# Performance work log

Measured on AMD Instinct MI355X. Metric: run time of the kernel, lower is better.

Reference implementation:

```python
import jax, jax.numpy as jnp
import numpy as np

H = 64

def _lstm_cell(x, h, c, Wih, Whh, bih, bhh):
    # x: [B, in], h/c: [B, H]; gate order i, f, g, o (PyTorch convention)
    g = x @ Wih.T + h @ Whh.T + (bih + bhh)
    i, f, gg, o = jnp.split(g, 4, axis=-1)
    i = jax.nn.sigmoid(i)
    f = jax.nn.sigmoid(f)
    gg = jnp.tanh(gg)
    o = jax.nn.sigmoid(o)
    c_new = f * c + i * gg
    h_new = o * jnp.tanh(c_new)
    return h_new, c_new


def setup_inputs() -> dict:
    key = jax.random.key(0)
    ks = jax.random.split(key, 12)
    B, T = 512, 1024
    s1 = 1.0 / np.sqrt(H)
    u = lambda k, shape: jax.random.uniform(k, shape, jnp.float32, -s1, s1)
    return {
        "x": jax.random.normal(ks[0], (B, T), jnp.float32),
        "W_ih1": u(ks[1], (4 * H, 1)),
        "W_hh1": u(ks[2], (4 * H, H)),
        "b_ih1": u(ks[3], (4 * H,)),
        "b_hh1": u(ks[4], (4 * H,)),
        "W_ih2": u(ks[5], (4 * H, H)),
        "W_hh2": u(ks[6], (4 * H, H)),
        "b_ih2": u(ks[7], (4 * H,)),
        "b_hh2": u(ks[8], (4 * H,)),
        "W_l": u(ks[9], (1, H)),
        "b_l": u(ks[10], (1,)),
        "future": 64,
    }


def reference(x, W_ih1, W_hh1, b_ih1, b_hh1, W_ih2, W_hh2, b_ih2, b_hh2, W_l, b_l, future):
    B, T = x.shape
    h1 = jnp.zeros((B, H), jnp.float32)
    c1 = jnp.zeros((B, H), jnp.float32)
    h2 = jnp.zeros((B, H), jnp.float32)
    c2 = jnp.zeros((B, H), jnp.float32)

    def step(carry, xt):
        h1, c1, h2, c2 = carry
        h1, c1 = _lstm_cell(xt, h1, c1, W_ih1, W_hh1, b_ih1, b_hh1)
        h2, c2 = _lstm_cell(h1, h2, c2, W_ih2, W_hh2, b_ih2, b_hh2)
        out = h2 @ W_l.T + b_l  # [B, 1]
        return (h1, c1, h2, c2), out

    xs = x.T[:, :, None]  # [T, B, 1]
    (h1, c1, h2, c2), outs = jax.lax.scan(step, (h1, c1, h2, c2), xs)
    last_out = outs[-1]  # [B, 1]

    def fstep(carry, _):
        h1, c1, h2, c2, out = carry
        h1, c1 = _lstm_cell(out, h1, c1, W_ih1, W_hh1, b_ih1, b_hh1)
        h2, c2 = _lstm_cell(h1, h2, c2, W_ih2, W_hh2, b_ih2, b_hh2)
        out = h2 @ W_l.T + b_l
        return (h1, c1, h2, c2, out), out

    if future > 0:
        _, fouts = jax.lax.scan(fstep, (h1, c1, h2, c2, last_out), None, length=future)
        outs = jnp.concatenate([outs, fouts], axis=0)  # [T+future, B, 1]

    return outs[:, :, 0].T  # [B, T+future]
```

## Files before the change

kernel.cpp:

```cpp
#include <hip/hip_runtime.h>

#define TMAIN 1024
#define TFUT  64
#define TTOT  (TMAIN + TFUT)

#define RL(v,k) __uint_as_float(__builtin_amdgcn_readlane(__float_as_uint(v),(k)))
#define DPPF(v,ctrl) __int_as_float(__builtin_amdgcn_update_dpp(0, __float_as_int(v), (ctrl), 0xf, 0xf, true))
#define DPPADD(d,ctrl,rm) d += __int_as_float(__builtin_amdgcn_update_dpp(0, __float_as_int(d), (ctrl), (rm), 0xf, true));

#define LD16(N,P) \
  float4 N##0=(P)[0],  N##1=(P)[1],  N##2=(P)[2],  N##3=(P)[3],  \
         N##4=(P)[4],  N##5=(P)[5],  N##6=(P)[6],  N##7=(P)[7],  \
         N##8=(P)[8],  N##9=(P)[9],  N##10=(P)[10], N##11=(P)[11], \
         N##12=(P)[12], N##13=(P)[13], N##14=(P)[14], N##15=(P)[15];

#define PIN(v) asm volatile("" : "+v"(v.x), "+v"(v.y), "+v"(v.z), "+v"(v.w));
#define PIN16(N) PIN(N##0) PIN(N##1) PIN(N##2) PIN(N##3) PIN(N##4) PIN(N##5) PIN(N##6) PIN(N##7) \
                 PIN(N##8) PIN(N##9) PIN(N##10) PIN(N##11) PIN(N##12) PIN(N##13) PIN(N##14) PIN(N##15)

#define D4(W,k,hv) \
  a0 = fmaf(RL(hv,(k)+0), W.x, a0); \
  a1 = fmaf(RL(hv,(k)+1), W.y, a1); \
  a2 = fmaf(RL(hv,(k)+2), W.z, a2); \
  a3 = fmaf(RL(hv,(k)+3), W.w, a3);

#define DOT64(N,hv) \
  D4(N##0,0,hv)   D4(N##1,4,hv)   D4(N##2,8,hv)   D4(N##3,12,hv)  \
  D4(N##4,16,hv)  D4(N##5,20,hv)  D4(N##6,24,hv)  D4(N##7,28,hv)  \
  D4(N##8,32,hv)  D4(N##9,36,hv)  D4(N##10,40,hv) D4(N##11,44,hv) \
  D4(N##12,48,hv) D4(N##13,52,hv) D4(N##14,56,hv) D4(N##15,60,hv)

__global__ __launch_bounds__(256, 2)
void lstm2_kernel(const float* __restrict__ x,
                  const float* __restrict__ Wih1,
                  const float* __restrict__ Whh1,
                  const float* __restrict__ bih1,
                  const float* __restrict__ bhh1,
                  const float* __restrict__ Wih2,
                  const float* __restrict__ Whh2,
                  const float* __restrict__ bih2,
                  const float* __restrict__ bhh2,
                  const float* __restrict__ Wl,
                  const float* __restrict__ bl,
                  float* __restrict__ out)
{
    const int b    = blockIdx.x;
    const int tid  = threadIdx.x;
    const int wv   = tid >> 6;
    const int lane = tid & 63;
    const int q    = lane & 3;
    const int unit = (wv << 4) | (lane >> 2);
    const int row  = (q << 6) | unit;

    LD16(A, reinterpret_cast<const float4*>(Whh1 + row * 64))
    LD16(C, reinterpret_cast<const float4*>(Wih2 + row * 64))
    LD16(D, reinterpret_cast<const float4*>(Whh2 + row * 64))
    PIN16(A) PIN16(C) PIN16(D)

    const float wih1r = Wih1[row];
    const float bias1 = bih1[row] + bhh1[row];
    const float bias2 = bih2[row] + bhh2[row];
    const float wl_l  = Wl[lane];
    const float bl0   = bl[0];

    __shared__ float h1buf[64];
    __shared__ float h2buf[64];

    float vh1o = 0.0f, vh2o = 0.0f, c1 = 0.0f, c2 = 0.0f, xv = 0.0f;
    const float* xb = x + b * TMAIN;
    float* ob = out + b * TTOT;

    for (int s = 0; s < TTOT; ++s) {
        const float x_t = (s < TMAIN) ? xb[s] : xv;

        float a0 = 0.f, a1 = 0.f, a2 = 0.f, a3 = 0.f;
        DOT64(A, vh1o)
        float acc = fmaf(wih1r, x_t, bias1) + ((a0 + a1) + (a2 + a3));

        float earg = (q == 2) ? -2.0f * acc : -acc;
        float r  = 1.0f / (1.0f + __expf(earg));
        float gv = (q == 2) ? 2.0f * r - 1.0f : r;
        float p1v = DPPF(gv, 0xB1);
        float p2v = DPPF(gv, 0x4E);
        float p3v = DPPF(gv, 0x1B);
        float gi = (q==0)?gv : (q==1)?p1v : (q==2)?p2v : p3v;
        float gf = (q==1)?gv : (q==0)?p1v : (q==3)?p2v : p3v;
        float gg = (q==2)?gv : (q==3)?p1v : (q==0)?p2v : p3v;
        float go = (q==3)?gv : (q==2)?p1v : (q==1)?p2v : p3v;
        c1 = fmaf(gf, c1, gi * gg);
        float tr = 1.0f / (1.0f + __expf(-2.0f * c1));
        float h1n = go * (2.0f * tr - 1.0f);
        if (q == 0) h1buf[unit] = h1n;
        __syncthreads();
        const float vh1n = h1buf[lane];

        a0 = 0.f; a1 = 0.f; a2 = 0.f; a3 = 0.f;
        DOT64(C, vh1n)
        DOT64(D, vh2o)
        acc = bias2 + ((a0 + a1) + (a2 + a3));
        earg = (q == 2) ? -2.0f * acc : -acc;
        r  = 1.0f / (1.0f + __expf(earg));
        gv = (q == 2) ? 2.0f * r - 1.0f : r;
        p1v = DPPF(gv, 0xB1); p2v = DPPF(gv, 0x4E); p3v = DPPF(gv, 0x1B);
        gi = (q==0)?gv : (q==1)?p1v : (q==2)?p2v : p3v;
        gf = (q==1)?gv : (q==0)?p1v : (q==3)?p2v : p3v;
        gg = (q==2)?gv : (q==3)?p1v : (q==0)?p2v : p3v;
        go = (q==3)?gv : (q==2)?p1v : (q==1)?p2v : p3v;
        c2 = fmaf(gf, c2, gi * gg);
        tr = 1.0f / (1.0f + __expf(-2.0f * c2));
        float h2n = go * (2.0f * tr - 1.0f);
        if (q == 0) h2buf[unit] = h2n;
        __syncthreads();
        const float vh2n = h2buf[lane];

        float rs = wl_l * vh2n;
        DPPADD(rs, 0x111, 0xf)
        DPPADD(rs, 0x112, 0xf)
        DPPADD(rs, 0x114, 0xf)
        DPPADD(rs, 0x118, 0xf)
        DPPADD(rs, 0x142, 0xa)
        DPPADD(rs, 0x143, 0xc)
        xv = RL(rs, 63) + bl0;
        if (tid == 0) ob[s] = xv;

        vh1o = vh1n;
        vh2o = vh2n;
    }
}

extern "C" void kernel_launch(void* const* d_in, const int* in_sizes, int n_in,
                              void* d_out, int out_size, void* d_ws, size_t ws_size,
                              hipStream_t stream)
{
    const float* xx   = (const float*)d_in[0];
    const float* Wih1 = (const float*)d_in[1];
    const float* Whh1 = (const float*)d_in[2];
    const float* bih1 = (const float*)d_in[3];
    const float* bhh1 = (const float*)d_in[4];
    const float* Wih2 = (const float*)d_in[5];
    const float* Whh2 = (const float*)d_in[6];
    const float* bih2 = (const float*)d_in[7];
    const float* bhh2 = (const float*)d_in[8];
    const float* Wl   = (const float*)d_in[9];
    const float* bl   = (const float*)d_in[10];
    float* out = (float*)d_out;

    lstm2_kernel<<<dim3(512), dim3(256), 0, stream>>>(
        xx, Wih1, Whh1, bih1, bhh1, Wih2, Whh2, bih2, bhh2, Wl, bl, out);
}
```

Baseline: 2.285 ms.

## Split LSTM hidden-dim reductions across two wave halves and overlap layer-2 recurrent matvec

```diff
diff --git a/kernel.cpp b/kernel.cpp
--- a/kernel.cpp
+++ b/kernel.cpp
@@ -8,29 +8,22 @@
 #define DPPF(v,ctrl) __int_as_float(__builtin_amdgcn_update_dpp(0, __float_as_int(v), (ctrl), 0xf, 0xf, true))
 #define DPPADD(d,ctrl,rm) d += __int_as_float(__builtin_amdgcn_update_dpp(0, __float_as_int(d), (ctrl), (rm), 0xf, true));
 
-#define LD16(N,P) \
-  float4 N##0=(P)[0],  N##1=(P)[1],  N##2=(P)[2],  N##3=(P)[3],  \
-         N##4=(P)[4],  N##5=(P)[5],  N##6=(P)[6],  N##7=(P)[7],  \
-         N##8=(P)[8],  N##9=(P)[9],  N##10=(P)[10], N##11=(P)[11], \
-         N##12=(P)[12], N##13=(P)[13], N##14=(P)[14], N##15=(P)[15];
-
+#define LD8(N,P) \
+  float4 N##0=(P)[0], N##1=(P)[1], N##2=(P)[2], N##3=(P)[3], \
+         N##4=(P)[4], N##5=(P)[5], N##6=(P)[6], N##7=(P)[7];
 #define PIN(v) asm volatile("" : "+v"(v.x), "+v"(v.y), "+v"(v.z), "+v"(v.w));
-#define PIN16(N) PIN(N##0) PIN(N##1) PIN(N##2) PIN(N##3) PIN(N##4) PIN(N##5) PIN(N##6) PIN(N##7) \
-                 PIN(N##8) PIN(N##9) PIN(N##10) PIN(N##11) PIN(N##12) PIN(N##13) PIN(N##14) PIN(N##15)
+#define PIN8(N) PIN(N##0) PIN(N##1) PIN(N##2) PIN(N##3) PIN(N##4) PIN(N##5) PIN(N##6) PIN(N##7)
 
 #define D4(W,k,hv) \
   a0 = fmaf(RL(hv,(k)+0), W.x, a0); \
   a1 = fmaf(RL(hv,(k)+1), W.y, a1); \
   a2 = fmaf(RL(hv,(k)+2), W.z, a2); \
   a3 = fmaf(RL(hv,(k)+3), W.w, a3);
+#define DOT32(N,hv) \
+  D4(N##0,0,hv)  D4(N##1,4,hv)  D4(N##2,8,hv)  D4(N##3,12,hv) \
+  D4(N##4,16,hv) D4(N##5,20,hv) D4(N##6,24,hv) D4(N##7,28,hv)
 
-#define DOT64(N,hv) \
-  D4(N##0,0,hv)   D4(N##1,4,hv)   D4(N##2,8,hv)   D4(N##3,12,hv)  \
-  D4(N##4,16,hv)  D4(N##5,20,hv)  D4(N##6,24,hv)  D4(N##7,28,hv)  \
-  D4(N##8,32,hv)  D4(N##9,36,hv)  D4(N##10,40,hv) D4(N##11,44,hv) \
-  D4(N##12,48,hv) D4(N##13,52,hv) D4(N##14,56,hv) D4(N##15,60,hv)
-
-__global__ __launch_bounds__(256, 2)
+__global__ __launch_bounds__(512, 4)
 void lstm2_kernel(const float* __restrict__ x,
                   const float* __restrict__ Wih1,
                   const float* __restrict__ Whh1,
@@ -46,16 +39,20 @@
 {
     const int b    = blockIdx.x;
     const int tid  = threadIdx.x;
-    const int wv   = tid >> 6;
+    const int half = tid >> 8;
     const int lane = tid & 63;
+    const int wq   = (tid >> 6) & 3;
     const int q    = lane & 3;
-    const int unit = (wv << 4) | (lane >> 2);
+    const int unit = (wq << 4) | (lane >> 2);
     const int row  = (q << 6) | unit;
+    const int pidx = (unit << 2) | q;
+    const int koff = half << 5;
 
-    LD16(A, reinterpret_cast<const float4*>(Whh1 + row * 64))
-    LD16(C, reinterpret_cast<const float4*>(Wih2 + row * 64))
-    LD16(D, reinterpret_cast<const float4*>(Whh2 + row * 64))
-    PIN16(A) PIN16(C) PIN16(D)
+    const float4* pA = reinterpret_cast<const float4*>(Whh1 + row * 64 + koff);
+    const float4* pB = reinterpret_cast<const float4*>(Wih2 + row * 64 + koff);
+    const float4* pC = reinterpret_cast<const float4*>(Whh2 + row * 64 + koff);
+    LD8(A, pA) LD8(B, pB) LD8(C, pC)
+    PIN8(A) PIN8(B) PIN8(C)
 
     const float wih1r = Wih1[row];
     const float bias1 = bih1[row] + bhh1[row];
@@ -63,68 +60,77 @@
     const float wl_l  = Wl[lane];
     const float bl0   = bl[0];
 
-    __shared__ float h1buf[64];
-    __shared__ float h2buf[64];
+    __shared__ float part1[256], part2[256], part3[256];
+    __shared__ float h1buf[64], h2buf[64];
 
-    float vh1o = 0.0f, vh2o = 0.0f, c1 = 0.0f, c2 = 0.0f, xv = 0.0f;
+    float vh1 = 0.f, vh2 = 0.f, c1 = 0.f, c2 = 0.f, xv = 0.f;
     const float* xb = x + b * TMAIN;
     float* ob = out + b * TTOT;
 
     for (int s = 0; s < TTOT; ++s) {
-        const float x_t = (s < TMAIN) ? xb[s] : xv;
+        float a0 = 0.f, a1 = 0.f, a2 = 0.f, a3 = 0.f;
+        DOT32(A, vh1)
+        const float p1 = (a0 + a1) + (a2 + a3);
+        a0 = 0.f; a1 = 0.f; a2 = 0.f; a3 = 0.f;
+        DOT32(C, vh2)
+        const float p2 = (a0 + a1) + (a2 + a3);
+        if (half) { part1[pidx] = p1; part2[pidx] = p2; }
+        __syncthreads();
 
-        float a0 = 0.f, a1 = 0.f, a2 = 0.f, a3 = 0.f;
-        DOT64(A, vh1o)
-        float acc = fmaf(wih1r, x_t, bias1) + ((a0 + a1) + (a2 + a3));
-
-        float earg = (q == 2) ? -2.0f * acc : -acc;
-        float r  = 1.0f / (1.0f + __expf(earg));
-        float gv = (q == 2) ? 2.0f * r - 1.0f : r;
-        float p1v = DPPF(gv, 0xB1);
-        float p2v = DPPF(gv, 0x4E);
-        float p3v = DPPF(gv, 0x1B);
-        float gi = (q==0)?gv : (q==1)?p1v : (q==2)?p2v : p3v;
-        float gf = (q==1)?gv : (q==0)?p1v : (q==3)?p2v : p3v;
-        float gg = (q==2)?gv : (q==3)?p1v : (q==0)?p2v : p3v;
-        float go = (q==3)?gv : (q==2)?p1v : (q==1)?p2v : p3v;
-        c1 = fmaf(gf, c1, gi * gg);
-        float tr = 1.0f / (1.0f + __expf(-2.0f * c1));
-        float h1n = go * (2.0f * tr - 1.0f);
-        if (q == 0) h1buf[unit] = h1n;
+        if (!half) {
+            const float x_t = (s < TMAIN) ? xb[s] : xv;
+            float acc = p1 + part1[pidx] + fmaf(wih1r, x_t, bias1);
+            float earg = (q == 2) ? -2.f * acc : -acc;
+            float r  = __builtin_amdgcn_rcpf(1.f + __expf(earg));
+            float gv = (q == 2) ? fmaf(2.f, r, -1.f) : r;
+            float u1 = DPPF(gv, 0xB1), u2 = DPPF(gv, 0x4E), u3 = DPPF(gv, 0x1B);
+            float gi = (q==0)?gv : (q==1)?u1 : (q==2)?u2 : u3;
+            float gf = (q==1)?gv : (q==0)?u1 : (q==3)?u2 : u3;
+            float gg = (q==2)?gv : (q==3)?u1 : (q==0)?u2 : u3;
+            float go = (q==3)?gv : (q==2)?u1 : (q==1)?u2 : u3;
+            c1 = fmaf(gf, c1, gi * gg);
+            float tr = __builtin_amdgcn_rcpf(1.f + __expf(-2.f * c1));
+            float h1n = go * fmaf(2.f, tr, -1.f);
+            if (q == 0) h1buf[unit] = h1n;
+        }
         __syncthreads();
-        const float vh1n = h1buf[lane];
+        vh1 = h1buf[(lane + koff) & 63];
 
         a0 = 0.f; a1 = 0.f; a2 = 0.f; a3 = 0.f;
-        DOT64(C, vh1n)
-        DOT64(D, vh2o)
-        acc = bias2 + ((a0 + a1) + (a2 + a3));
-        earg = (q == 2) ? -2.0f * acc : -acc;
-        r  = 1.0f / (1.0f + __expf(earg));
-        gv = (q == 2) ? 2.0f * r - 1.0f : r;
-        p1v = DPPF(gv, 0xB1); p2v = DPPF(gv, 0x4E); p3v = DPPF(gv, 0x1B);
-        gi = (q==0)?gv : (q==1)?p1v : (q==2)?p2v : p3v;
-        gf = (q==1)?gv : (q==0)?p1v : (q==3)?p2v : p3v;
-        gg = (q==2)?gv : (q==3)?p1v : (q==0)?p2v : p3v;
-        go = (q==3)?gv : (q==2)?p1v : (q==1)?p2v : p3v;
-        c2 = fmaf(gf, c2, gi * gg);
-        tr = 1.0f / (1.0f + __expf(-2.0f * c2));
-        float h2n = go * (2.0f * tr - 1.0f);
-        if (q == 0) h2buf[unit] = h2n;
+        DOT32(B, vh1)
+        const float p3 = (a0 + a1) + (a2 + a3);
+        if (half) part3[pidx] = p3;
         __syncthreads();
-        const float vh2n = h2buf[lane];
 
-        float rs = wl_l * vh2n;
-        DPPADD(rs, 0x111, 0xf)
-        DPPADD(rs, 0x112, 0xf)
-        DPPADD(rs, 0x114, 0xf)
-        DPPADD(rs, 0x118, 0xf)
-        DPPADD(rs, 0x142, 0xa)
-        DPPADD(rs, 0x143, 0xc)
-        xv = RL(rs, 63) + bl0;
-        if (tid == 0) ob[s] = xv;
+        if (!half) {
+            float acc = p2 + part2[pidx] + p3 + part3[pidx] + bias2;
+            float earg = (q == 2) ? -2.f * acc : -acc;
+            float r  = __builtin_amdgcn_rcpf(1.f + __expf(earg));
+            float gv = (q == 2) ? fmaf(2.f, r, -1.f) : r;
+            float u1 = DPPF(gv, 0xB1), u2 = DPPF(gv, 0x4E), u3 = DPPF(gv, 0x1B);
+            float gi = (q==0)?gv : (q==1)?u1 : (q==2)?u2 : u3;
+            float gf = (q==1)?gv : (q==0)?u1 : (q==3)?u2 : u3;
+            float gg = (q==2)?gv : (q==3)?u1 : (q==0)?u2 : u3;
+            float go = (q==3)?gv : (q==2)?u1 : (q==1)?u2 : u3;
+            c2 = fmaf(gf, c2, gi * gg);
+            float tr = __builtin_amdgcn_rcpf(1.f + __expf(-2.f * c2));
+            float h2n = go * fmaf(2.f, tr, -1.f);
+            if (q == 0) h2buf[unit] = h2n;
+        }
+        __syncthreads();
+        vh2 = h2buf[(lane + koff) & 63];
 
-        vh1o = vh1n;
-        vh2o = vh2n;
+        if (!half) {
+            float rs = wl_l * vh2;
+            DPPADD(rs, 0x111, 0xf)
+            DPPADD(rs, 0x112, 0xf)
+            DPPADD(rs, 0x114, 0xf)
+            DPPADD(rs, 0x118, 0xf)
+            DPPADD(rs, 0x142, 0xa)
+            DPPADD(rs, 0x143, 0xc)
+            xv = RL(rs, 63) + bl0;
+            if (tid == 0) ob[s] = xv;
+        }
     }
 }
 
@@ -145,6 +151,6 @@
     const float* bl   = (const float*)d_in[10];
     float* out = (float*)d_out;
 
-    lstm2_kernel<<<dim3(512), dim3(256), 0, stream>>>(
+    lstm2_kernel<<<dim3(512), dim3(512), 0, stream>>>(
         xx, Wih1, Whh1, bih1, bhh1, Wih2, Whh2, bih2, bhh2, Wl, bl, out);
 }
```

Result: slower. 2.373 ms (+3.9%).
